# Kernel tuning notes

Measured on AMD Instinct MI355X. Metric: run time of the kernel, lower is better.

The kernel has to match this reference:

```python
import jax, jax.numpy as jnp
import numpy as np

N_LAYERS = 6
N_HEADS = 16
D_MODEL = 1024
D_HEAD = D_MODEL // N_HEADS
D_FF = 4096
VOCAB = 32000
MAX_LEN = 1024
B, T = 2, 1024
NEG = -1e9
EPS = 1e-5


def layernorm(x, s, b):
    mu = jnp.mean(x, axis=-1, keepdims=True)
    var = jnp.mean(jnp.square(x - mu), axis=-1, keepdims=True)
    return (x - mu) * jax.lax.rsqrt(var + EPS) * s + b


def setup_inputs() -> dict:
    key = jax.random.key(0)
    ks = jax.random.split(key, 8)
    s = 0.02
    return {
        "idx": jax.random.randint(ks[0], (B, T), 0, VOCAB),
        "tok_emb": jax.random.normal(ks[1], (VOCAB, D_MODEL), jnp.float32) * s,
        "pos_emb": jax.random.normal(ks[2], (MAX_LEN, D_MODEL), jnp.float32) * s,
        "ln1_s": jnp.ones((N_LAYERS, D_MODEL), jnp.float32),
        "ln1_b": jnp.zeros((N_LAYERS, D_MODEL), jnp.float32),
        "qkv_w": jax.random.normal(ks[3], (N_LAYERS, D_MODEL, 3 * D_MODEL), jnp.float32) * s,
        "qkv_b": jnp.zeros((N_LAYERS, 3 * D_MODEL), jnp.float32),
        "out_w": jax.random.normal(ks[4], (N_LAYERS, D_MODEL, D_MODEL), jnp.float32) * s,
        "out_b": jnp.zeros((N_LAYERS, D_MODEL), jnp.float32),
        "ln2_s": jnp.ones((N_LAYERS, D_MODEL), jnp.float32),
        "ln2_b": jnp.zeros((N_LAYERS, D_MODEL), jnp.float32),
        "mlp_w1": jax.random.normal(ks[5], (N_LAYERS, D_MODEL, D_FF), jnp.float32) * s,
        "mlp_b1": jnp.zeros((N_LAYERS, D_FF), jnp.float32),
        "mlp_w2": jax.random.normal(ks[6], (N_LAYERS, D_FF, D_MODEL), jnp.float32) * s,
        "mlp_b2": jnp.zeros((N_LAYERS, D_MODEL), jnp.float32),
        "lnf_s": jnp.ones((D_MODEL,), jnp.float32),
        "lnf_b": jnp.zeros((D_MODEL,), jnp.float32),
        "head_w": jax.random.normal(ks[7], (D_MODEL, VOCAB), jnp.float32) * s,
    }


def reference(idx, tok_emb, pos_emb, ln1_s, ln1_b, qkv_w, qkv_b, out_w, out_b,
              ln2_s, ln2_b, mlp_w1, mlp_b1, mlp_w2, mlp_b2, lnf_s, lnf_b, head_w):
    b, t = idx.shape
    x = tok_emb[idx] + pos_emb[:t]  # [B,T,D]
    causal = jnp.tril(jnp.ones((t, t), dtype=bool))
    scale = 1.0 / np.sqrt(D_HEAD)
    for l in range(N_LAYERS):
        h = layernorm(x, ln1_s[l], ln1_b[l])
        qkv = h @ qkv_w[l] + qkv_b[l]  # [B,T,3D]
        q, k, v = jnp.split(qkv, 3, axis=-1)
        q = q.reshape(b, t, N_HEADS, D_HEAD).transpose(0, 2, 1, 3)
        k = k.reshape(b, t, N_HEADS, D_HEAD).transpose(0, 2, 1, 3)
        v = v.reshape(b, t, N_HEADS, D_HEAD).transpose(0, 2, 1, 3)
        att = jnp.einsum('bhqd,bhkd->bhqk', q, k) * scale
        att = jnp.where(causal, att, NEG)
        att = jax.nn.softmax(att, axis=-1)
        y = jnp.einsum('bhqk,bhkd->bhqd', att, v)
        y = y.transpose(0, 2, 1, 3).reshape(b, t, D_MODEL)
        x = x + (y @ out_w[l] + out_b[l])
        h = layernorm(x, ln2_s[l], ln2_b[l])
        m = jax.nn.gelu(h @ mlp_w1[l] + mlp_b1[l], approximate=False) @ mlp_w2[l] + mlp_b2[l]
        x = x + m
    x = layernorm(x, lnf_s, lnf_b)
    logits = x @ head_w  # [B,T,V]
    return logits
```

## Files before the change

kernel.cpp:

```cpp
#include <hip/hip_runtime.h>


#define T_SEQ 1024
#define NTOK  2048
#define DM    1024
#define DFF   4096
#define NH    16
#define DH    64
#define NL    6
#define VOCAB 32000

typedef short sx8 __attribute__((ext_vector_type(8)));
typedef float fx4 __attribute__((ext_vector_type(4)));
typedef unsigned short usx4 __attribute__((ext_vector_type(4)));
typedef unsigned int   uix4 __attribute__((ext_vector_type(4)));

__device__ __forceinline__ unsigned short f2bf(float f) {
  union { float f; unsigned u; } c; c.f = f;
  unsigned r = c.u + 0x7FFFu + ((c.u >> 16) & 1u);
  return (unsigned short)(r >> 16);
}

__device__ __forceinline__ void gload_lds16(const unsigned short* g, unsigned short* l) {
  __builtin_amdgcn_global_load_lds(
      (const __attribute__((address_space(1))) unsigned int*)g,
      (__attribute__((address_space(3))) unsigned int*)l, 16, 0, 0);
}

__device__ __forceinline__ int xcd_swizzle(int orig, int nwg) {
  int q = nwg >> 3, r = nwg & 7;
  int xcd = orig & 7, idx = orig >> 3;
  int base = (xcd < r) ? xcd * (q + 1) : r * (q + 1) + (xcd - r) * q;
  return base + idx;
}

__global__ __launch_bounds__(256) void k_embed(const int* __restrict__ idx,
                                               const float* __restrict__ tok,
                                               const float* __restrict__ pos,
                                               float* __restrict__ x) {
  int token = blockIdx.x;
  int t = token & (T_SEQ - 1);
  int id = idx[token];
  int c = threadIdx.x * 4;
  float4 tv = *(const float4*)&tok[(size_t)id * DM + c];
  float4 pv = *(const float4*)&pos[(size_t)t * DM + c];
  float4 r;
  r.x = tv.x + pv.x; r.y = tv.y + pv.y; r.z = tv.z + pv.z; r.w = tv.w + pv.w;
  *(float4*)&x[(size_t)token * DM + c] = r;
}

__global__ __launch_bounds__(256) void k_ln(const float* __restrict__ x,
                                            const float* __restrict__ g,
                                            const float* __restrict__ b,
                                            unsigned short* __restrict__ h) {
  int row = blockIdx.x;
  int tid = threadIdx.x;
  float4 v = *(const float4*)&x[(size_t)row * DM + tid * 4];
  float s = v.x + v.y + v.z + v.w;
  float q = v.x * v.x + v.y * v.y + v.z * v.z + v.w * v.w;
  for (int off = 32; off > 0; off >>= 1) {
    s += __shfl_down(s, off);
    q += __shfl_down(q, off);
  }
  __shared__ float red[8];
  int wid = tid >> 6, lane = tid & 63;
  if (lane == 0) { red[wid] = s; red[4 + wid] = q; }
  __syncthreads();
  s = red[0] + red[1] + red[2] + red[3];
  q = red[4] + red[5] + red[6] + red[7];
  float mu = s * (1.0f / DM);
  float var = q * (1.0f / DM) - mu * mu;
  float rstd = rsqrtf(var + 1e-5f);
  float4 gg = *(const float4*)&g[tid * 4];
  float4 bb = *(const float4*)&b[tid * 4];
  usx4 o;
  o[0] = f2bf((v.x - mu) * rstd * gg.x + bb.x);
  o[1] = f2bf((v.y - mu) * rstd * gg.y + bb.y);
  o[2] = f2bf((v.z - mu) * rstd * gg.z + bb.z);
  o[3] = f2bf((v.w - mu) * rstd * gg.w + bb.w);
  *(usx4*)&h[(size_t)row * DM + tid * 4] = o;
}

__global__ __launch_bounds__(256) void k_reduce_ln(const float* __restrict__ part,
                                                   float* __restrict__ x,
                                                   const float* __restrict__ g,
                                                   const float* __restrict__ b,
                                                   unsigned short* __restrict__ h) {
  int row = blockIdx.x;
  int tid = threadIdx.x;
  int c = tid * 4;
  float4 v = *(const float4*)&x[(size_t)row * DM + c];
#pragma unroll
  for (int s4 = 0; s4 < 4; ++s4) {
    float4 p = *(const float4*)&part[((size_t)s4 * NTOK + row) * DM + c];
    v.x += p.x; v.y += p.y; v.z += p.z; v.w += p.w;
  }
  *(float4*)&x[(size_t)row * DM + c] = v;
  float s = v.x + v.y + v.z + v.w;
  float q = v.x * v.x + v.y * v.y + v.z * v.z + v.w * v.w;
  for (int off = 32; off > 0; off >>= 1) {
    s += __shfl_down(s, off);
    q += __shfl_down(q, off);
  }
  __shared__ float red[8];
  int wid = tid >> 6, lane = tid & 63;
  if (lane == 0) { red[wid] = s; red[4 + wid] = q; }
  __syncthreads();
  s = red[0] + red[1] + red[2] + red[3];
  q = red[4] + red[5] + red[6] + red[7];
  float mu = s * (1.0f / DM);
  float var = q * (1.0f / DM) - mu * mu;
  float rstd = rsqrtf(var + 1e-5f);
  float4 gg = *(const float4*)&g[c];
  float4 bb = *(const float4*)&b[c];
  usx4 o;
  o[0] = f2bf((v.x - mu) * rstd * gg.x + bb.x);
  o[1] = f2bf((v.y - mu) * rstd * gg.y + bb.y);
  o[2] = f2bf((v.z - mu) * rstd * gg.z + bb.z);
  o[3] = f2bf((v.w - mu) * rstd * gg.w + bb.w);
  *(usx4*)&h[(size_t)row * DM + c] = o;
}

__global__ __launch_bounds__(256) void k_wtrans(const float* __restrict__ W,
                                                unsigned short* __restrict__ WT,
                                                int K, int N) {
  __shared__ float t[64][68];
  int k0 = blockIdx.x * 64, n0 = blockIdx.y * 64;
  int tid = threadIdx.x;
#pragma unroll
  for (int i = 0; i < 4; ++i) {
    int chunk = i * 256 + tid;
    int r = chunk >> 4, c = (chunk & 15) << 2;
    float4 v = *(const float4*)&W[(size_t)(k0 + r) * N + n0 + c];
    t[r][c] = v.x; t[r][c + 1] = v.y; t[r][c + 2] = v.z; t[r][c + 3] = v.w;
  }
  __syncthreads();
#pragma unroll
  for (int i = 0; i < 4; ++i) {
    int chunk = i * 256 + tid;
    int n = chunk >> 4, c = (chunk & 15) << 2;
    usx4 o;
    o[0] = f2bf(t[c][n]);
    o[1] = f2bf(t[c + 1][n]);
    o[2] = f2bf(t[c + 2][n]);
    o[3] = f2bf(t[c + 3][n]);
    *(usx4*)&WT[(size_t)(n0 + n) * K + k0 + c] = o;
  }
}

template <int EPI>
__global__ __launch_bounds__(256) void k_gemm(const unsigned short* __restrict__ A,
                                              const unsigned short* __restrict__ BT,
                                              const float* __restrict__ bias,
                                              float* __restrict__ part,
                                              unsigned short* __restrict__ outb,
                                              float* __restrict__ outf,
                                              int N, int K, int NT, int KS) {
  __shared__ unsigned short As[128 * 64];
  __shared__ unsigned short Bs[128 * 64];
  int tid = threadIdx.x;
  int wid = tid >> 6, lane = tid & 63;
  int lr = lane & 15, lg = lane >> 4;

  int id = xcd_swizzle(blockIdx.x, gridDim.x);
  int mt = id & 15;
  int rest = id >> 4;
  int nt = rest % NT;
  int ks = rest / NT;
  int m0 = mt * 128, n0 = nt * 128;
  int Kslice = K / KS;
  int kbeg = ks * Kslice, kend = kbeg + Kslice;

  int wm = (wid >> 1) * 64, wn = (wid & 1) * 64;

  fx4 acc[4][4] = {};

  for (int kt = kbeg; kt < kend; kt += 64) {
    __syncthreads();
#pragma unroll
    for (int i = 0; i < 4; ++i) {
      int chunk = i * 256 + tid;
      int r = chunk >> 3;
      int slot = chunk & 7;
      int c = ((slot ^ (r & 7)) << 3);
      gload_lds16(&A[(size_t)(m0 + r) * K + kt + c], &As[chunk << 3]);
      gload_lds16(&BT[(size_t)(n0 + r) * K + kt + c], &Bs[chunk << 3]);
    }
    __syncthreads();
#pragma unroll
    for (int kk = 0; kk < 2; ++kk) {
      int slotz = (kk * 4 + lg) ^ (lr & 7);
      sx8 fa[4], fb[4];
#pragma unroll
      for (int mi = 0; mi < 4; ++mi)
        fa[mi] = *(const sx8*)&As[(wm + mi * 16 + lr) * 64 + slotz * 8];
#pragma unroll
      for (int ni = 0; ni < 4; ++ni)
        fb[ni] = *(const sx8*)&Bs[(wn + ni * 16 + lr) * 64 + slotz * 8];
#pragma unroll
      for (int mi = 0; mi < 4; ++mi)
#pragma unroll
        for (int ni = 0; ni < 4; ++ni)
          acc[mi][ni] = __builtin_amdgcn_mfma_f32_16x16x32_bf16(fb[ni], fa[mi], acc[mi][ni], 0, 0, 0);
    }
  }

#pragma unroll
  for (int ni = 0; ni < 4; ++ni) {
    int col0 = n0 + wn + ni * 16 + lg * 4;
    float4 bv = {0.f, 0.f, 0.f, 0.f};
    if (bias && ks == 0) bv = *(const float4*)&bias[col0];
#pragma unroll
    for (int mi = 0; mi < 4; ++mi) {
      int row = m0 + wm + mi * 16 + lr;
      float v0 = acc[mi][ni][0] + bv.x;
      float v1 = acc[mi][ni][1] + bv.y;
      float v2 = acc[mi][ni][2] + bv.z;
      float v3 = acc[mi][ni][3] + bv.w;
      if constexpr (EPI == 0) {
        int bb = row >> 10, tt = row & 1023;
        if (col0 < 2048) {
          int which = col0 >> 10;
          int hc = col0 & 1023;
          usx4 o = {f2bf(v0), f2bf(v1), f2bf(v2), f2bf(v3)};
          *(usx4*)&outb[(size_t)which * NTOK * DM +
                        (((size_t)bb * NH + (hc >> 6)) * T_SEQ + tt) * DH + (hc & 63)] = o;
        } else {
          int dc = col0 - 2048;
          unsigned short* vt = outb + (size_t)2 * NTOK * DM;
          size_t base = (((size_t)bb * NH + (dc >> 6)) * DH + (dc & 63)) * T_SEQ + tt;
          vt[base] = f2bf(v0);
          vt[base + T_SEQ] = f2bf(v1);
          vt[base + 2 * T_SEQ] = f2bf(v2);
          vt[base + 3 * T_SEQ] = f2bf(v3);
        }
      } else if constexpr (EPI == 1) {
        usx4 o;
        o[0] = f2bf(0.5f * v0 * (1.0f + erff(v0 * 0.70710678f)));
        o[1] = f2bf(0.5f * v1 * (1.0f + erff(v1 * 0.70710678f)));
        o[2] = f2bf(0.5f * v2 * (1.0f + erff(v2 * 0.70710678f)));
        o[3] = f2bf(0.5f * v3 * (1.0f + erff(v3 * 0.70710678f)));
        *(usx4*)&outb[(size_t)row * N + col0] = o;
      } else {
        float4 o = {v0, v1, v2, v3};
        *(float4*)&part[((size_t)ks * NTOK + row) * DM + col0] = o;
      }
    }
  }
}

#define LDSUB(buf, ab, kk) (lds + (((buf) * 2 + (ab)) * 2 + (kk)) * 8192)

__device__ __forceinline__ void stage_half(const unsigned short* g, int rowstride,
                                           unsigned short* ldsbase, int tid, int k0) {
#pragma unroll
  for (int r = 0; r < 2; ++r) {
    int chunk = r * 512 + tid;
    int row = chunk >> 2, slot = chunk & 3;
    gload_lds16(g + (size_t)row * rowstride + k0 + ((slot ^ (row & 3)) << 3),
                ldsbase + (chunk << 3));
  }
}

__global__ __launch_bounds__(512, 2) void k_gemm256(const unsigned short* __restrict__ A,
                                                    const unsigned short* __restrict__ BT,
                                                    float* __restrict__ outf,
                                                    int N, int K) {
  __shared__ unsigned short lds[8 * 8192];
  int tid = threadIdx.x;
  int wid = tid >> 6, lane = tid & 63;
  int lr = lane & 15, lg = lane >> 4;
  int wm2 = wid >> 2, wn4 = wid & 3;
  int id = xcd_swizzle(blockIdx.x, gridDim.x);
  int mt = id & 7, nt = id >> 3;
  int m0 = mt * 256, n0 = nt * 256;
  const unsigned short* Ab = A + (size_t)m0 * K;
  const unsigned short* Bb = BT + (size_t)n0 * K;
  int NIT = K >> 7;
  int swz = (lg ^ (lr & 3)) << 3;

  fx4 acc[8][4] = {};

  stage_half(Ab, K, LDSUB(0, 0, 0), tid, 0);
  stage_half(Bb, K, LDSUB(0, 1, 0), tid, 0);
  stage_half(Ab, K, LDSUB(0, 0, 1), tid, 32);
  stage_half(Bb, K, LDSUB(0, 1, 1), tid, 32);
  stage_half(Ab, K, LDSUB(1, 0, 0), tid, 64);
  stage_half(Bb, K, LDSUB(1, 1, 0), tid, 64);
  stage_half(Ab, K, LDSUB(1, 0, 1), tid, 96);
  asm volatile("s_waitcnt vmcnt(6)" ::: "memory");
  __builtin_amdgcn_s_barrier();

#define PHASE(BUF, KK, NH, LOADA, STG, VMW)                                          \
  {                                                                                  \
    if (LOADA) {                                                                     \
      const unsigned short* sA = LDSUB(BUF, 0, KK);                                  \
      _Pragma("unroll")                                                              \
      for (int mi = 0; mi < 8; ++mi)                                                 \
        fa[mi] = *(const sx8*)&sA[(wm2 * 128 + mi * 16 + lr) * 32 + swz];            \
    }                                                                                \
    {                                                                                \
      const unsigned short* sB = LDSUB(BUF, 1, KK);                                  \
      _Pragma("unroll")                                                              \
      for (int j = 0; j < 2; ++j)                                                    \
        fb[j] = *(const sx8*)&sB[(wn4 * 64 + (NH) * 32 + j * 16 + lr) * 32 + swz];   \
    }                                                                                \
    STG;                                                                             \
    VMW;                                                                             \
    __builtin_amdgcn_sched_barrier(0);                                               \
    __builtin_amdgcn_s_barrier();                                                    \
    asm volatile("s_waitcnt lgkmcnt(0)" ::: "memory");                               \
    __builtin_amdgcn_sched_barrier(0);                                               \
    __builtin_amdgcn_s_setprio(1);                                                   \
    _Pragma("unroll")                                                                \
    for (int mi = 0; mi < 8; ++mi) {                                                 \
      acc[mi][(NH) * 2 + 0] = __builtin_amdgcn_mfma_f32_16x16x32_bf16(               \
          fb[0], fa[mi], acc[mi][(NH) * 2 + 0], 0, 0, 0);                            \
      acc[mi][(NH) * 2 + 1] = __builtin_amdgcn_mfma_f32_16x16x32_bf16(               \
          fb[1], fa[mi], acc[mi][(NH) * 2 + 1], 0, 0, 0);                            \
    }                                                                                \
    __builtin_amdgcn_s_setprio(0);                                                   \
    __builtin_amdgcn_sched_barrier(0);                                               \
    __builtin_amdgcn_s_barrier();                                                    \
  }

  for (int it = 0; it < NIT; ++it) {
    bool st = (it < NIT - 1);
    bool last = (it == NIT - 1);
    int t1k = (2 * it + 1) * 64;
    int t2k = (2 * it + 2) * 64;
    int t3k = (2 * it + 3) * 64;
    sx8 fa[8], fb[2];

    PHASE(0, 0, 0, true,
          { stage_half(Bb, K, LDSUB(1, 1, 1), tid, t1k + 32); }, {});
    PHASE(0, 0, 1, false,
          { if (st) stage_half(Ab, K, LDSUB(0, 0, 0), tid, t2k); }, {});
    PHASE(0, 1, 0, true,
          { if (st) stage_half(Bb, K, LDSUB(0, 1, 0), tid, t2k); }, {});
    PHASE(0, 1, 1, false,
          { if (st) stage_half(Ab, K, LDSUB(0, 0, 1), tid, t2k + 32); },
          { if (last) { asm volatile("s_waitcnt vmcnt(0)" ::: "memory"); }
            else      { asm volatile("s_waitcnt vmcnt(6)" ::: "memory"); } });
    PHASE(1, 0, 0, true,
          { if (st) stage_half(Bb, K, LDSUB(0, 1, 1), tid, t2k + 32); }, {});
    PHASE(1, 0, 1, false,
          { if (st) stage_half(Ab, K, LDSUB(1, 0, 0), tid, t3k); }, {});
    PHASE(1, 1, 0, true,
          { if (st) stage_half(Bb, K, LDSUB(1, 1, 0), tid, t3k); }, {});
    PHASE(1, 1, 1, false,
          { if (st) stage_half(Ab, K, LDSUB(1, 0, 1), tid, t3k + 32); },
          { if (!last) { asm volatile("s_waitcnt vmcnt(6)" ::: "memory"); } });
  }
#undef PHASE

#pragma unroll
  for (int mi = 0; mi < 8; ++mi) {
    int row = m0 + wm2 * 128 + mi * 16 + lr;
    float* orow = outf + (size_t)row * N + n0 + wn4 * 64 + lg * 4;
#pragma unroll
    for (int nj = 0; nj < 4; ++nj) {
      float4 o = {acc[mi][nj][0], acc[mi][nj][1], acc[mi][nj][2], acc[mi][nj][3]};
      *(float4*)&orow[nj * 16] = o;
    }
  }
}

__global__ __launch_bounds__(256) void k_attn(const unsigned short* __restrict__ gq,
                                              const unsigned short* __restrict__ gk,
                                              const unsigned short* __restrict__ gvt,
                                              unsigned short* __restrict__ y) {
  __shared__ unsigned short Ks[128 * 64];
  __shared__ unsigned short Vt[64 * 128];
  __shared__ unsigned short Pw[4][16 * 136];
  int id = xcd_swizzle(blockIdx.x, gridDim.x);
  int bh = id >> 4, qt = 15 - (id & 15);
  int tid = threadIdx.x, wid = tid >> 6, lane = tid & 63;
  int lr = lane & 15, lg = lane >> 4;
  int q0 = qt * 64 + wid * 16;
  int qg = q0 + lr;

  sx8 qf[2];
  {
    const unsigned short* qp = gq + ((size_t)bh * T_SEQ + qg) * DH + lg * 8;
    qf[0] = *(const sx8*)qp;
    qf[1] = *(const sx8*)(qp + 32);
  }

  fx4 yacc[4] = {};
  float mrun = -1e30f, lrun = 0.f;

  int jmax = qt >> 1;
  for (int j = 0; j <= jmax; ++j) {
    int kt0 = j * 128;
    __syncthreads();
#pragma unroll
    for (int i = 0; i < 4; ++i) {
      int chunk = i * 256 + tid;
      {
        int r = chunk >> 3, s = chunk & 7;
        gload_lds16(&gk[((size_t)bh * T_SEQ + kt0 + r) * DH + ((s ^ (r & 7)) << 3)],
                    &Ks[chunk << 3]);
      }
      {
        int r = chunk >> 4, s = chunk & 15;
        gload_lds16(&gvt[((size_t)bh * DH + r) * T_SEQ + kt0 + ((s ^ (r & 15)) << 3)],
                    &Vt[chunk << 3]);
      }
    }
    __syncthreads();

    fx4 st[8] = {};
#pragma unroll
    for (int kk = 0; kk < 2; ++kk) {
      int slotz = (kk * 4 + lg) ^ (lr & 7);
#pragma unroll
      for (int mi = 0; mi < 8; ++mi) {
        sx8 kb = *(const sx8*)&Ks[(mi * 16 + lr) * 64 + slotz * 8];
        st[mi] = __builtin_amdgcn_mfma_f32_16x16x32_bf16(kb, qf[kk], st[mi], 0, 0, 0);
      }
    }

    float pvv[8][4];
    float pmax = -1e30f;
    bool lastj = (j == jmax);
#pragma unroll
    for (int mi = 0; mi < 8; ++mi)
#pragma unroll
      for (int rg = 0; rg < 4; ++rg) {
        float val = st[mi][rg] * 0.125f;
        if (lastj && (kt0 + mi * 16 + lg * 4 + rg) > qg) val = -1e30f;
        pvv[mi][rg] = val;
        pmax = fmaxf(pmax, val);
      }
    pmax = fmaxf(pmax, __shfl_xor(pmax, 16));
    pmax = fmaxf(pmax, __shfl_xor(pmax, 32));
    if (!__all(pmax <= mrun + 8.0f)) {
      float mnew = fmaxf(mrun, pmax);
      float sc = __expf(mrun - mnew);
      lrun *= sc;
#pragma unroll
      for (int dt = 0; dt < 4; ++dt)
#pragma unroll
        for (int rg = 0; rg < 4; ++rg) yacc[dt][rg] *= sc;
      mrun = mnew;
    }
    float ps = 0.f;
#pragma unroll
    for (int mi = 0; mi < 8; ++mi)
#pragma unroll
      for (int rg = 0; rg < 4; ++rg) {
        float e = __expf(pvv[mi][rg] - mrun);
        pvv[mi][rg] = e;
        ps += e;
      }
    ps += __shfl_xor(ps, 16);
    ps += __shfl_xor(ps, 32);
    lrun += ps;

#pragma unroll
    for (int mi = 0; mi < 8; ++mi)
#pragma unroll
      for (int rp = 0; rp < 2; ++rp) {
        unsigned pk = (unsigned)f2bf(pvv[mi][rp * 2]) |
                      ((unsigned)f2bf(pvv[mi][rp * 2 + 1]) << 16);
        *(unsigned*)&Pw[wid][lr * 136 + mi * 16 + lg * 4 + rp * 2] = pk;
      }

#pragma unroll
    for (int kk = 0; kk < 4; ++kk) {
      sx8 pa = *(const sx8*)&Pw[wid][lr * 136 + kk * 32 + lg * 8];
      int slotz = (kk * 4 + lg) ^ lr;
#pragma unroll
      for (int dt = 0; dt < 4; ++dt) {
        sx8 vb = *(const sx8*)&Vt[(dt * 16 + lr) * 128 + slotz * 8];
        yacc[dt] = __builtin_amdgcn_mfma_f32_16x16x32_bf16(vb, pa, yacc[dt], 0, 0, 0);
      }
    }
  }

  float inv = 1.0f / lrun;
  int tok = (bh >> 4) * T_SEQ + qg;
  int colbase = (bh & 15) * DH;
#pragma unroll
  for (int dt = 0; dt < 4; ++dt) {
    usx4 o;
#pragma unroll
    for (int rg = 0; rg < 4; ++rg) o[rg] = f2bf(yacc[dt][rg] * inv);
    *(usx4*)&y[(size_t)tok * DM + colbase + dt * 16 + lg * 4] = o;
  }
}

extern "C" void kernel_launch(void* const* d_in, const int* in_sizes, int n_in,
                              void* d_out, int out_size, void* d_ws, size_t ws_size,
                              hipStream_t stream) {
  (void)in_sizes; (void)n_in; (void)out_size; (void)ws_size;
  const int*   idx     = (const int*)d_in[0];
  const float* tok_emb = (const float*)d_in[1];
  const float* pos_emb = (const float*)d_in[2];
  const float* ln1_s   = (const float*)d_in[3];
  const float* ln1_b   = (const float*)d_in[4];
  const float* qkv_w   = (const float*)d_in[5];
  const float* qkv_b   = (const float*)d_in[6];
  const float* out_w   = (const float*)d_in[7];
  const float* out_b   = (const float*)d_in[8];
  const float* ln2_s   = (const float*)d_in[9];
  const float* ln2_b   = (const float*)d_in[10];
  const float* mlp_w1  = (const float*)d_in[11];
  const float* mlp_b1  = (const float*)d_in[12];
  const float* mlp_w2  = (const float*)d_in[13];
  const float* mlp_b2  = (const float*)d_in[14];
  const float* lnf_s   = (const float*)d_in[15];
  const float* lnf_b   = (const float*)d_in[16];
  const float* head_w  = (const float*)d_in[17];

  char* p = (char*)d_ws;
  float* x          = (float*)p;          p += (size_t)NTOK * DM * 4;
  unsigned short* h = (unsigned short*)p; p += (size_t)NTOK * DM * 2;
  unsigned short* qkvb = (unsigned short*)p; p += (size_t)3 * NTOK * DM * 2;
  unsigned short* yb = (unsigned short*)p; p += (size_t)NTOK * DM * 2;
  unsigned short* m1 = (unsigned short*)p; p += (size_t)NTOK * DFF * 2;
  unsigned short* wt = (unsigned short*)p;
  float* part = (float*)(p + 32 * 1024 * 1024);

  dim3 blk(256);

  k_embed<<<NTOK, blk, 0, stream>>>(idx, tok_emb, pos_emb, x);
  k_ln<<<NTOK, blk, 0, stream>>>(x, ln1_s, ln1_b, h);

  for (int l = 0; l < NL; ++l) {
    k_wtrans<<<dim3(DM / 64, 3 * DM / 64), blk, 0, stream>>>(qkv_w + (size_t)l * DM * 3 * DM, wt, DM, 3 * DM);
    k_gemm<0><<<16 * 24, blk, 0, stream>>>(h, wt, qkv_b + l * 3 * DM,
                                           nullptr, qkvb, nullptr, 3 * DM, DM, 24, 1);
    k_attn<<<512, blk, 0, stream>>>(qkvb, qkvb + (size_t)NTOK * DM,
                                    qkvb + (size_t)2 * NTOK * DM, yb);
    k_wtrans<<<dim3(DM / 64, DM / 64), blk, 0, stream>>>(out_w + (size_t)l * DM * DM, wt, DM, DM);
    k_gemm<2><<<16 * 8 * 4, blk, 0, stream>>>(yb, wt, out_b + l * DM,
                                              part, nullptr, nullptr, DM, DM, 8, 4);
    k_reduce_ln<<<NTOK, blk, 0, stream>>>(part, x, ln2_s + l * DM, ln2_b + l * DM, h);
    k_wtrans<<<dim3(DM / 64, DFF / 64), blk, 0, stream>>>(mlp_w1 + (size_t)l * DM * DFF, wt, DM, DFF);
    k_gemm<1><<<16 * 32, blk, 0, stream>>>(h, wt, mlp_b1 + l * DFF,
                                           nullptr, m1, nullptr, DFF, DM, 32, 1);
    k_wtrans<<<dim3(DFF / 64, DM / 64), blk, 0, stream>>>(mlp_w2 + (size_t)l * DFF * DM, wt, DFF, DM);
    k_gemm<2><<<16 * 8 * 4, blk, 0, stream>>>(m1, wt, mlp_b2 + l * DM,
                                              part, nullptr, nullptr, DM, DFF, 8, 4);
    if (l < NL - 1)
      k_reduce_ln<<<NTOK, blk, 0, stream>>>(part, x, ln1_s + (l + 1) * DM, ln1_b + (l + 1) * DM, h);
    else
      k_reduce_ln<<<NTOK, blk, 0, stream>>>(part, x, lnf_s, lnf_b, h);
  }

  k_wtrans<<<dim3(DM / 64, VOCAB / 64), blk, 0, stream>>>(head_w, wt, DM, VOCAB);
  k_gemm256<<<1000, 512, 0, stream>>>(h, wt, (float*)d_out, VOCAB, DM);
}
```

Baseline: 1.217 ms.

## Store split-K partials in bf16, retune LDS swizzle, use exp2 softmax

```diff
diff --git a/kernel.cpp b/kernel.cpp
--- a/kernel.cpp
+++ b/kernel.cpp
@@ -19,6 +19,10 @@
   union { float f; unsigned u; } c; c.f = f;
   unsigned r = c.u + 0x7FFFu + ((c.u >> 16) & 1u);
   return (unsigned short)(r >> 16);
+}
+__device__ __forceinline__ float bf2f(unsigned short u) {
+  union { unsigned u; float f; } c; c.u = ((unsigned)u) << 16;
+  return c.f;
 }
 
 __device__ __forceinline__ void gload_lds16(const unsigned short* g, unsigned short* l) {
@@ -81,7 +85,7 @@
   *(usx4*)&h[(size_t)row * DM + tid * 4] = o;
 }
 
-__global__ __launch_bounds__(256) void k_reduce_ln(const float* __restrict__ part,
+__global__ __launch_bounds__(256) void k_reduce_ln(const unsigned short* __restrict__ part,
                                                    float* __restrict__ x,
                                                    const float* __restrict__ g,
                                                    const float* __restrict__ b,
@@ -92,8 +96,8 @@
   float4 v = *(const float4*)&x[(size_t)row * DM + c];
 #pragma unroll
   for (int s4 = 0; s4 < 4; ++s4) {
-    float4 p = *(const float4*)&part[((size_t)s4 * NTOK + row) * DM + c];
-    v.x += p.x; v.y += p.y; v.z += p.z; v.w += p.w;
+    usx4 p = *(const usx4*)&part[((size_t)s4 * NTOK + row) * DM + c];
+    v.x += bf2f(p[0]); v.y += bf2f(p[1]); v.z += bf2f(p[2]); v.w += bf2f(p[3]);
   }
   *(float4*)&x[(size_t)row * DM + c] = v;
   float s = v.x + v.y + v.z + v.w;
@@ -152,7 +156,7 @@
 __global__ __launch_bounds__(256) void k_gemm(const unsigned short* __restrict__ A,
                                               const unsigned short* __restrict__ BT,
                                               const float* __restrict__ bias,
-                                              float* __restrict__ part,
+                                              unsigned short* __restrict__ part,
                                               unsigned short* __restrict__ outb,
                                               float* __restrict__ outf,
                                               int N, int K, int NT, int KS) {
@@ -242,8 +246,8 @@
         o[3] = f2bf(0.5f * v3 * (1.0f + erff(v3 * 0.70710678f)));
         *(usx4*)&outb[(size_t)row * N + col0] = o;
       } else {
-        float4 o = {v0, v1, v2, v3};
-        *(float4*)&part[((size_t)ks * NTOK + row) * DM + col0] = o;
+        usx4 o = {f2bf(v0), f2bf(v1), f2bf(v2), f2bf(v3)};
+        *(usx4*)&part[((size_t)ks * NTOK + row) * DM + col0] = o;
       }
     }
   }
@@ -257,7 +261,7 @@
   for (int r = 0; r < 2; ++r) {
     int chunk = r * 512 + tid;
     int row = chunk >> 2, slot = chunk & 3;
-    gload_lds16(g + (size_t)row * rowstride + k0 + ((slot ^ (row & 3)) << 3),
+    gload_lds16(g + (size_t)row * rowstride + k0 + ((slot ^ ((row >> 1) & 3)) << 3),
                 ldsbase + (chunk << 3));
   }
 }
@@ -277,7 +281,7 @@
   const unsigned short* Ab = A + (size_t)m0 * K;
   const unsigned short* Bb = BT + (size_t)n0 * K;
   int NIT = K >> 7;
-  int swz = (lg ^ (lr & 3)) << 3;
+  int swz = (lg ^ ((lr >> 1) & 3)) << 3;
 
   fx4 acc[8][4] = {};
 
@@ -291,7 +295,7 @@
   asm volatile("s_waitcnt vmcnt(6)" ::: "memory");
   __builtin_amdgcn_s_barrier();
 
-#define PHASE(BUF, KK, NH, LOADA, STG, VMW)                                          \
+#define PHASE(BUF, KK, NHH, LOADA, STG, VMW)                                         \
   {                                                                                  \
     if (LOADA) {                                                                     \
       const unsigned short* sA = LDSUB(BUF, 0, KK);                                  \
@@ -303,7 +307,7 @@
       const unsigned short* sB = LDSUB(BUF, 1, KK);                                  \
       _Pragma("unroll")                                                              \
       for (int j = 0; j < 2; ++j)                                                    \
-        fb[j] = *(const sx8*)&sB[(wn4 * 64 + (NH) * 32 + j * 16 + lr) * 32 + swz];   \
+        fb[j] = *(const sx8*)&sB[(wn4 * 64 + (NHH) * 32 + j * 16 + lr) * 32 + swz];  \
     }                                                                                \
     STG;                                                                             \
     VMW;                                                                             \
@@ -314,10 +318,10 @@
     __builtin_amdgcn_s_setprio(1);                                                   \
     _Pragma("unroll")                                                                \
     for (int mi = 0; mi < 8; ++mi) {                                                 \
-      acc[mi][(NH) * 2 + 0] = __builtin_amdgcn_mfma_f32_16x16x32_bf16(               \
-          fb[0], fa[mi], acc[mi][(NH) * 2 + 0], 0, 0, 0);                            \
-      acc[mi][(NH) * 2 + 1] = __builtin_amdgcn_mfma_f32_16x16x32_bf16(               \
-          fb[1], fa[mi], acc[mi][(NH) * 2 + 1], 0, 0, 0);                            \
+      acc[mi][(NHH) * 2 + 0] = __builtin_amdgcn_mfma_f32_16x16x32_bf16(              \
+          fb[0], fa[mi], acc[mi][(NHH) * 2 + 0], 0, 0, 0);                           \
+      acc[mi][(NHH) * 2 + 1] = __builtin_amdgcn_mfma_f32_16x16x32_bf16(              \
+          fb[1], fa[mi], acc[mi][(NHH) * 2 + 1], 0, 0, 0);                           \
     }                                                                                \
     __builtin_amdgcn_s_setprio(0);                                                   \
     __builtin_amdgcn_sched_barrier(0);                                               \
@@ -379,6 +383,7 @@
   int lr = lane & 15, lg = lane >> 4;
   int q0 = qt * 64 + wid * 16;
   int qg = q0 + lr;
+  const float SCL = 0.125f * 1.44269504f;
 
   sx8 qf[2];
   {
@@ -428,16 +433,16 @@
     for (int mi = 0; mi < 8; ++mi)
 #pragma unroll
       for (int rg = 0; rg < 4; ++rg) {
-        float val = st[mi][rg] * 0.125f;
+        float val = st[mi][rg] * SCL;
         if (lastj && (kt0 + mi * 16 + lg * 4 + rg) > qg) val = -1e30f;
         pvv[mi][rg] = val;
         pmax = fmaxf(pmax, val);
       }
     pmax = fmaxf(pmax, __shfl_xor(pmax, 16));
     pmax = fmaxf(pmax, __shfl_xor(pmax, 32));
-    if (!__all(pmax <= mrun + 8.0f)) {
+    if (!__all(pmax <= mrun + 11.5f)) {
       float mnew = fmaxf(mrun, pmax);
-      float sc = __expf(mrun - mnew);
+      float sc = exp2f(mrun - mnew);
       lrun *= sc;
 #pragma unroll
       for (int dt = 0; dt < 4; ++dt)
@@ -450,7 +455,7 @@
     for (int mi = 0; mi < 8; ++mi)
 #pragma unroll
       for (int rg = 0; rg < 4; ++rg) {
-        float e = __expf(pvv[mi][rg] - mrun);
+        float e = exp2f(pvv[mi][rg] - mrun);
         pvv[mi][rg] = e;
         ps += e;
       }
@@ -521,7 +526,7 @@
   unsigned short* yb = (unsigned short*)p; p += (size_t)NTOK * DM * 2;
   unsigned short* m1 = (unsigned short*)p; p += (size_t)NTOK * DFF * 2;
   unsigned short* wt = (unsigned short*)p;
-  float* part = (float*)(p + 32 * 1024 * 1024);
+  unsigned short* part = (unsigned short*)(p + 32 * 1024 * 1024);
 
   dim3 blk(256);
 
```

Result: faster. 1.182 ms (-2.9%).
